# Optimization experiments

Measured on AMD Instinct MI355X. Metric: run time of the kernel, lower is better.

## Reference

```python
import jax, jax.numpy as jnp
import numpy as np

B, E, DM = 2, 1024, 512          # batch, n_edges, d_model
H, DK, DV = 8, 64, 64            # heads, d_k, d_v
MAX_NEIGHBOR = 5                 # == attn_max_dist
LN_EPS = 1e-6
NEG = -1e9


def setup_inputs() -> dict:
    key = jax.random.key(0)
    ks = jax.random.split(key, 9)
    s = 0.02
    return {
        "x": jax.random.normal(ks[0], (B, DM, E, 1), jnp.float32),
        "dist": jax.random.randint(ks[1], (B, E, E), 0, 12, jnp.int32),
        "base_rpr": jax.random.normal(ks[2], (MAX_NEIGHBOR + 1, DK), jnp.float32) * s,
        "w_q": jax.random.normal(ks[3], (DM, H * DK), jnp.float32) * s,
        "w_k": jax.random.normal(ks[4], (DM, H * DK), jnp.float32) * s,
        "w_v": jax.random.normal(ks[5], (DM, H * DV), jnp.float32) * s,
        "w_fc": jax.random.normal(ks[6], (H * DV, DM), jnp.float32) * s,
        "ln_g": jnp.ones((DM,), jnp.float32),
        "ln_b": jnp.zeros((DM,), jnp.float32),
    }


def reference(x, dist, base_rpr, w_q, w_k, w_v, w_fc, ln_g, ln_b):
    temp = jnp.asarray(DK, x.dtype) ** 0.5
    # local-attention mask (dist <= attn_max_dist); all edges valid (same-size meshes)
    mask = dist <= MAX_NEIGHBOR                      # [B,E,E] bool

    s = jnp.transpose(x[..., 0], (0, 2, 1))          # [B,E,DM]
    residual = s

    # LayerNorm applied to q only (as in the torch module)
    mu = s.mean(-1, keepdims=True)
    var = ((s - mu) ** 2).mean(-1, keepdims=True)
    qn = (s - mu) / jnp.sqrt(var + LN_EPS) * ln_g + ln_b

    q = (qn @ w_q).reshape(B, E, H, DK).transpose(0, 2, 1, 3)   # [B,H,E,DK]
    k = (s @ w_k).reshape(B, E, H, DK).transpose(0, 2, 1, 3)
    v = (s @ w_v).reshape(B, E, H, DV).transpose(0, 2, 1, 3)

    # relative-position representations gathered by (clipped) distance
    rpr = base_rpr[jnp.minimum(dist, MAX_NEIGHBOR)]  # [B,E,E,DK]

    qs = q / temp
    attn1 = jnp.einsum("bhid,bhjd->bhij", qs, k)
    attn2 = jnp.einsum("bhid,bijd->bhij", qs, rpr)
    logits = jnp.where(mask[:, None], attn1 + attn2, NEG)
    attn = jax.nn.softmax(logits, axis=-1)           # [B,H,E,E]

    out = jnp.einsum("bhij,bhjd->bhid", attn, v)     # [B,H,E,DV]
    out = out.transpose(0, 2, 1, 3).reshape(B, E, H * DV) @ w_fc + residual
    x_out = out.transpose(0, 2, 1)[..., None]        # [B,DM,E,1]

    mf = mask[:, None].astype(attn.dtype)            # [B,1,E,E]
    attn_per_edge = (attn * mf).sum((1, 2)) / mf.sum((1, 2))  # [B,E]
    return x_out, attn, attn_per_edge
```

## Files before the change

### kernel.cpp

```cpp
#include <hip/hip_runtime.h>

#define NB_B 2
#define NB_E 1024
#define NB_DM 512
#define NB_H 8

typedef __attribute__((ext_vector_type(8))) __bf16 bf16x8;
typedef __attribute__((ext_vector_type(8))) unsigned short u16x8;
typedef __attribute__((ext_vector_type(4))) float f32x4;

static __device__ __forceinline__ float bf2f(unsigned short u){
  union { unsigned int i; float f; } v; v.i = ((unsigned int)u) << 16; return v.f;
}
static __device__ __forceinline__ unsigned short f2bf(float f){
  union { float f; unsigned int i; } v; v.f = f;
  unsigned int r = v.i + 0x7FFFu + ((v.i >> 16) & 1u);
  return (unsigned short)(r >> 16);
}
static __device__ __forceinline__ f32x4 mfma16(bf16x8 a, bf16x8 b, f32x4 c){
  return __builtin_amdgcn_mfma_f32_16x16x32_bf16(a, b, c, 0, 0, 0);
}
static __device__ __forceinline__ float fast_exp2(float x){
#if __has_builtin(__builtin_amdgcn_exp2f)
  return __builtin_amdgcn_exp2f(x);
#else
  return exp2f(x);
#endif
}

__global__ void k_transpose_x(const float* __restrict__ x, unsigned short* __restrict__ s_bf){
  __shared__ float tile[32][33];
  const int b = blockIdx.z;
  const int d0 = blockIdx.y * 32;
  const int e0 = blockIdx.x * 32;
  const int tx = threadIdx.x, ty = threadIdx.y;
  #pragma unroll
  for (int r = 0; r < 4; ++r){
    const int d = d0 + ty + r*8;
    tile[ty + r*8][tx] = x[((size_t)b*NB_DM + d)*NB_E + e0 + tx];
  }
  __syncthreads();
  #pragma unroll
  for (int r = 0; r < 4; ++r){
    const int e = e0 + ty + r*8;
    s_bf[((size_t)b*NB_E + e)*NB_DM + d0 + tx] = f2bf(tile[tx][ty + r*8]);
  }
}

__global__ void k_transpose_w(const float* __restrict__ w0, const float* __restrict__ w1,
                              const float* __restrict__ w2, const float* __restrict__ w3,
                              unsigned short* __restrict__ wT){
  __shared__ float tile[32][33];
  const int which = blockIdx.z;
  const float* w = which==0 ? w0 : which==1 ? w1 : which==2 ? w2 : w3;
  unsigned short* dst = wT + (size_t)which*512*512;
  const int k0 = blockIdx.y*32, n0 = blockIdx.x*32;
  const int tx = threadIdx.x, ty = threadIdx.y;
  #pragma unroll
  for (int r = 0; r < 4; ++r)
    tile[ty + r*8][tx] = w[(size_t)(k0 + ty + r*8)*512 + n0 + tx];
  __syncthreads();
  #pragma unroll
  for (int r = 0; r < 4; ++r)
    dst[(size_t)(n0 + ty + r*8)*512 + k0 + tx] = f2bf(tile[tx][ty + r*8]);
}

__global__ __launch_bounds__(256) void k_ln(const unsigned short* __restrict__ s_bf,
    unsigned short* __restrict__ qn_bf, const float* __restrict__ gg, const float* __restrict__ bb){
  const int row = blockIdx.x*4 + (threadIdx.x >> 6);
  const int l = threadIdx.x & 63;
  const unsigned short* sp = s_bf + (size_t)row*512 + l*8;
  u16x8 v = *(const u16x8*)sp;
  float f[8]; float sum = 0.f, sq = 0.f;
  #pragma unroll
  for (int i = 0; i < 8; ++i){ f[i] = bf2f(v[i]); sum += f[i]; sq += f[i]*f[i]; }
  #pragma unroll
  for (int off = 32; off >= 1; off >>= 1){
    sum += __shfl_xor(sum, off);
    sq  += __shfl_xor(sq, off);
  }
  const float mu  = sum * (1.f/512.f);
  const float var = sq * (1.f/512.f) - mu*mu;
  const float rstd = rsqrtf(var + 1e-6f);
  const float4 g0 = *(const float4*)(gg + l*8);
  const float4 g1 = *(const float4*)(gg + l*8 + 4);
  const float4 b0 = *(const float4*)(bb + l*8);
  const float4 b1 = *(const float4*)(bb + l*8 + 4);
  const float gv[8] = {g0.x,g0.y,g0.z,g0.w,g1.x,g1.y,g1.z,g1.w};
  const float bv[8] = {b0.x,b0.y,b0.z,b0.w,b1.x,b1.y,b1.z,b1.w};
  u16x8 o;
  #pragma unroll
  for (int i = 0; i < 8; ++i) o[i] = f2bf((f[i]-mu)*rstd*gv[i] + bv[i]);
  *(u16x8*)(qn_bf + (size_t)row*512 + l*8) = o;
}

__global__ __launch_bounds__(256) void k_dist(const int* __restrict__ dist,
    unsigned char* __restrict__ d8, int* __restrict__ cnt){
  const int b = blockIdx.y;
  const int i0 = blockIdx.x * 16;
  const int t = threadIdx.x;
  int c0 = 0, c1 = 0, c2 = 0, c3 = 0;
  #pragma unroll 4
  for (int r = 0; r < 16; ++r){
    const int row = i0 + r;
    const int4 d = ((const int4*)(dist + ((size_t)b*NB_E + row)*NB_E))[t];
    uchar4 o;
    o.x = (unsigned char)(d.x <= 5 ? d.x : 6);
    o.y = (unsigned char)(d.y <= 5 ? d.y : 6);
    o.z = (unsigned char)(d.z <= 5 ? d.z : 6);
    o.w = (unsigned char)(d.w <= 5 ? d.w : 6);
    ((uchar4*)(d8 + ((size_t)b*NB_E + row)*NB_E))[t] = o;
    c0 += (d.x <= 5); c1 += (d.y <= 5); c2 += (d.z <= 5); c3 += (d.w <= 5);
  }
  int* cb = cnt + b*NB_E + t*4;
  atomicAdd(cb + 0, c0);
  atomicAdd(cb + 1, c1);
  atomicAdd(cb + 2, c2);
  atomicAdd(cb + 3, c3);
}

__global__ __launch_bounds__(256, 4) void k_gemm_qkv(
    const unsigned short* __restrict__ qn, const unsigned short* __restrict__ s,
    const unsigned short* __restrict__ wT, const float* __restrict__ base_rpr,
    unsigned short* __restrict__ Qb, unsigned short* __restrict__ Kb,
    unsigned short* __restrict__ VTb, float* __restrict__ qr)
{
  const int z = blockIdx.z;
  const unsigned short* A  = (z == 0) ? qn : s;
  const unsigned short* BT = wT + (size_t)z*262144;
  const int tid = threadIdx.x;
  const int l = tid & 63, wv = tid >> 6;
  const int ll = l & 15, lg = l >> 4;
  const int m0 = blockIdx.x*64 + wv*16;
  const int n0 = blockIdx.y*64;
  const unsigned short* arow = A + (size_t)(m0 + ll)*512 + lg*8;
  const unsigned short* brow = BT + (size_t)(n0 + ll)*512 + lg*8;
  f32x4 acc[4];
  #pragma unroll
  for (int nt = 0; nt < 4; ++nt) acc[nt] = (f32x4){0.f,0.f,0.f,0.f};
  bf16x8 a_c = *(const bf16x8*)(arow);
  bf16x8 b_c[4];
  #pragma unroll
  for (int nt = 0; nt < 4; ++nt) b_c[nt] = *(const bf16x8*)(brow + (size_t)nt*8192);
  #pragma unroll
  for (int ks = 0; ks < 16; ++ks){
    const int kn = (ks + 1) & 15;
    bf16x8 a_n = *(const bf16x8*)(arow + kn*32);
    bf16x8 b_n[4];
    #pragma unroll
    for (int nt = 0; nt < 4; ++nt) b_n[nt] = *(const bf16x8*)(brow + (size_t)nt*8192 + kn*32);
    #pragma unroll
    for (int nt = 0; nt < 4; ++nt) acc[nt] = mfma16(a_c, b_c[nt], acc[nt]);
    a_c = a_n;
    #pragma unroll
    for (int nt = 0; nt < 4; ++nt) b_c[nt] = b_n[nt];
  }
  const int rbase = m0 + lg*4;
  const int bidx = rbase >> 10;
  const int e = rbase & 1023;
  const int h = n0 >> 6;
  if (z == 0){
    float rprv[6][4];
    #pragma unroll
    for (int c = 0; c < 6; ++c)
      #pragma unroll
      for (int nt = 0; nt < 4; ++nt)
        rprv[c][nt] = base_rpr[c*64 + nt*16 + ll];
    #pragma unroll
    for (int nt = 0; nt < 4; ++nt){
      const int dk = nt*16 + ll;
      unsigned short* dp = Qb + (((size_t)bidx*NB_H + h)*NB_E + e)*64 + dk;
      #pragma unroll
      for (int r = 0; r < 4; ++r)
        dp[(size_t)r*64] = f2bf(acc[nt][r]*0.125f);
    }
    #pragma unroll
    for (int r = 0; r < 4; ++r){
      #pragma unroll
      for (int c = 0; c < 6; ++c){
        float tv = 0.f;
        #pragma unroll
        for (int nt = 0; nt < 4; ++nt) tv += acc[nt][r]*0.125f*rprv[c][nt];
        tv += __shfl_xor(tv, 1);
        tv += __shfl_xor(tv, 2);
        tv += __shfl_xor(tv, 4);
        tv += __shfl_xor(tv, 8);
        if (ll == 0)
          qr[(((size_t)(bidx*NB_H + h)*NB_E) + e + r)*8 + c] = tv;
      }
    }
  } else if (z == 1){
    #pragma unroll
    for (int nt = 0; nt < 4; ++nt){
      const int dk = nt*16 + ll;
      unsigned short* dp = Kb + (((size_t)bidx*NB_H + h)*NB_E + e)*64 + dk;
      #pragma unroll
      for (int r = 0; r < 4; ++r)
        dp[(size_t)r*64] = f2bf(acc[nt][r]);
    }
  } else {
    #pragma unroll
    for (int nt = 0; nt < 4; ++nt){
      const int dv = nt*16 + ll;
      ushort4 ov;
      ov.x = f2bf(acc[nt][0]); ov.y = f2bf(acc[nt][1]);
      ov.z = f2bf(acc[nt][2]); ov.w = f2bf(acc[nt][3]);
      *(ushort4*)(VTb + (((size_t)bidx*NB_H + h)*64 + dv)*NB_E + e) = ov;
    }
  }
}

__global__ __launch_bounds__(256, 4) void k_fc(
    const unsigned short* __restrict__ A, const unsigned short* __restrict__ BT,
    float* __restrict__ dst_f, const float* __restrict__ resid)
{
  const int tid = threadIdx.x;
  const int l = tid & 63, wv = tid >> 6;
  const int ll = l & 15, lg = l >> 4;
  const int m0 = blockIdx.x*64 + wv*16;
  const int n0 = blockIdx.y*32;
  const unsigned short* arow = A + (size_t)(m0 + ll)*512 + lg*8;
  const unsigned short* brow = BT + (size_t)(n0 + ll)*512 + lg*8;
  f32x4 acc[2];
  acc[0] = (f32x4){0.f,0.f,0.f,0.f};
  acc[1] = (f32x4){0.f,0.f,0.f,0.f};
  bf16x8 a_c = *(const bf16x8*)(arow);
  bf16x8 b_c0 = *(const bf16x8*)(brow);
  bf16x8 b_c1 = *(const bf16x8*)(brow + 8192);
  #pragma unroll
  for (int ks = 0; ks < 16; ++ks){
    const int kn = (ks + 1) & 15;
    bf16x8 a_n  = *(const bf16x8*)(arow + kn*32);
    bf16x8 b_n0 = *(const bf16x8*)(brow + kn*32);
    bf16x8 b_n1 = *(const bf16x8*)(brow + 8192 + kn*32);
    acc[0] = mfma16(a_c, b_c0, acc[0]);
    acc[1] = mfma16(a_c, b_c1, acc[1]);
    a_c = a_n; b_c0 = b_n0; b_c1 = b_n1;
  }
  const int rbase = m0 + lg*4;
  const int bidx = rbase >> 10;
  const int e = rbase & 1023;
  #pragma unroll
  for (int nt = 0; nt < 2; ++nt){
    const int n = n0 + nt*16 + ll;
    const float* xr = resid + ((size_t)bidx*NB_DM + n)*NB_E + e;
    const float4 rv = *(const float4*)xr;
    const float4 ov = make_float4(acc[nt][0]+rv.x, acc[nt][1]+rv.y,
                                  acc[nt][2]+rv.z, acc[nt][3]+rv.w);
    *(float4*)(dst_f + ((size_t)bidx*NB_DM + n)*NB_E + e) = ov;
  }
}

#define D_OFF 1024
#define P_OFF 10240
__global__ __launch_bounds__(512, 8) void k_attn(
    const unsigned short* __restrict__ Q, const unsigned short* __restrict__ K,
    const unsigned short* __restrict__ VT, const float* __restrict__ qr,
    const unsigned char* __restrict__ d8, float* __restrict__ attn_out,
    unsigned short* __restrict__ outb, float* __restrict__ apeacc16)
{
  __shared__ __align__(16) unsigned char smem[26624];
  unsigned short* plds = (unsigned short*)(smem + P_OFF);
  float* qr_l = (float*)smem;
  float* reds = (float*)(smem + 256);

  const int tid = threadIdx.x;
  const int l = tid & 63, w = tid >> 6;
  const int lg = l >> 4, ll = l & 15;
  const int n = blockIdx.x;
  const int m = n >> 3;
  const int bh = (n & 7)*2 + (m >> 7);
  const int b = bh >> 3;
  const int ib = (m & 127) << 3;
  const int j0 = w << 7;

  const unsigned char* d8g = d8 + ((size_t)b*NB_E + ib)*NB_E;
  const int4 dr0 = ((const int4*)d8g)[tid];
  ((int4*)(smem + D_OFF))[tid] = dr0;

  if (tid < 48)
    qr_l[tid] = qr[((size_t)bh*NB_E + ib + (tid/6))*8 + (tid % 6)];

  const unsigned short* Qbp = Q + ((size_t)bh*NB_E + ib)*64;
  bf16x8 qf0 = *(const bf16x8*)(Qbp + (size_t)(ll & 7)*64 + lg*8);
  bf16x8 qf1 = *(const bf16x8*)(Qbp + (size_t)(ll & 7)*64 + 32 + lg*8);

  f32x4 s[8];
  const unsigned short* Kb = K + (size_t)bh*NB_E*64;
  #pragma unroll
  for (int jt = 0; jt < 8; ++jt){
    const size_t krow = (size_t)(j0 + jt*16 + ll)*64;
    bf16x8 k0 = *(const bf16x8*)(Kb + krow + lg*8);
    bf16x8 k1 = *(const bf16x8*)(Kb + krow + 32 + lg*8);
    f32x4 acc = {0.f,0.f,0.f,0.f};
    acc = mfma16(qf0, k0, acc);
    acc = mfma16(qf1, k1, acc);
    s[jt] = acc;
  }
  __syncthreads();

  if (lg < 2){
    float rsum[4] = {0.f, 0.f, 0.f, 0.f};
    #pragma unroll
    for (int jt = 0; jt < 8; ++jt){
      const int j = j0 + jt*16 + ll;
      #pragma unroll
      for (int r = 0; r < 4; ++r){
        const int il = lg*4 + r;
        const unsigned char c = smem[D_OFF + il*1024 + j];
        const float p = (c < 6)
          ? fast_exp2((s[jt][r] + qr_l[il*6 + c]) * 1.4426950408889634f) : 0.f;
        s[jt][r] = p;
        rsum[r] += p;
      }
    }
    #pragma unroll
    for (int r = 0; r < 4; ++r){
      float sum = rsum[r];
      sum += __shfl_xor(sum, 1);
      sum += __shfl_xor(sum, 2);
      sum += __shfl_xor(sum, 4);
      sum += __shfl_xor(sum, 8);
      if (ll == 0) reds[w*8 + lg*4 + r] = sum;
    }
  }
  __syncthreads();

  if (lg < 2){
    float rinv[4];
    #pragma unroll
    for (int r = 0; r < 4; ++r){
      const int il = lg*4 + r;
      float tot = 0.f;
      #pragma unroll
      for (int wv = 0; wv < 8; ++wv) tot += reds[wv*8 + il];
      rinv[r] = 1.0f / (tot + 1e-30f);
    }
    #pragma unroll
    for (int jt = 0; jt < 8; ++jt){
      const int j = j0 + jt*16 + ll;
      float csum = 0.f;
      #pragma unroll
      for (int r = 0; r < 4; ++r){
        const int il = lg*4 + r;
        const float pn = s[jt][r] * rinv[r];
        const int byo = ((il*1024 + j)*2) ^ (il << 4);
        plds[byo >> 1] = f2bf(pn);
        csum += pn;
      }
      csum += __shfl_xor(csum, 16);
      if (lg == 0) atomicAdd(&apeacc16[(bh << 10) + j], csum);
    }
  }
  __syncthreads();

  if (w < 4){
    const unsigned short* Vb = VT + ((size_t)bh*64 + w*16 + ll)*NB_E;
    f32x4 o = {0.f,0.f,0.f,0.f};
    #pragma unroll 4
    for (int kk = 0; kk < 32; ++kk){
      bf16x8 vf = *(const bf16x8*)(Vb + kk*32 + lg*8);
      const int byo = (((ll & 7)*1024 + kk*32 + lg*8)*2) ^ ((ll & 7) << 4);
      bf16x8 p = *(const bf16x8*)(smem + P_OFF + byo);
      o = mfma16(p, vf, o);
    }
    if (lg < 2){
      const int coln = (bh & 7)*64 + w*16 + ll;
      #pragma unroll
      for (int r = 0; r < 4; ++r){
        const int e0 = ib + lg*4 + r;
        outb[((size_t)b*NB_E + e0)*512 + coln] = f2bf(o[r]);
      }
    }
  }

  {
    float* arow = attn_out + ((size_t)bh*NB_E + ib + w)*NB_E;
    #pragma unroll
    for (int c2 = 0; c2 < 4; ++c2){
      const int col = c2*256 + l*4;
      const int byo = ((w*1024 + col)*2) ^ (w << 4);
      const ushort4 pv = *(const ushort4*)(smem + P_OFF + byo);
      f32x4 ov;
      ov[0] = bf2f(pv.x); ov[1] = bf2f(pv.y); ov[2] = bf2f(pv.z); ov[3] = bf2f(pv.w);
      *(f32x4*)(arow + col) = ov;
    }
  }
}

__global__ void k_ape(const float* __restrict__ acc, const int* __restrict__ cnt,
                      float* __restrict__ out){
  const int t = blockIdx.x*256 + threadIdx.x;
  if (t < NB_B*NB_E){
    const int b = t >> 10, j = t & 1023;
    float ssum = 0.f;
    #pragma unroll
    for (int h = 0; h < 8; ++h) ssum += acc[(((b<<3) + h) << 10) + j];
    const int c = cnt[t];
    out[t] = c > 0 ? ssum / (float)c : 0.f;
  }
}

extern "C" void kernel_launch(void* const* d_in, const int* in_sizes, int n_in,
                              void* d_out, int out_size, void* d_ws, size_t ws_size,
                              hipStream_t stream)
{
  const float* x        = (const float*)d_in[0];
  const int*   dist     = (const int*)d_in[1];
  const float* base_rpr = (const float*)d_in[2];
  const float* w_q      = (const float*)d_in[3];
  const float* w_k      = (const float*)d_in[4];
  const float* w_v      = (const float*)d_in[5];
  const float* w_fc     = (const float*)d_in[6];
  const float* ln_g     = (const float*)d_in[7];
  const float* ln_b     = (const float*)d_in[8];

  float* x_out    = (float*)d_out;
  float* attn_out = x_out + (size_t)NB_B*NB_DM*NB_E;
  float* ape_out  = attn_out + (size_t)NB_B*NB_H*NB_E*NB_E;

  unsigned char* ws = (unsigned char*)d_ws;
  unsigned short* s_bf   = (unsigned short*)(ws);
  unsigned short* qn_bf  = (unsigned short*)(ws + 2097152);
  unsigned short* wT     = (unsigned short*)(ws + 4194304);
  unsigned short* Qb     = (unsigned short*)(ws + 6291456);
  unsigned short* Kb     = (unsigned short*)(ws + 8388608);
  unsigned short* VTb    = (unsigned short*)(ws + 10485760);
  unsigned short* outb   = (unsigned short*)(ws + 12582912);
  float*          qr     = (float*)(ws + 14680064);
  unsigned char*  d8     = ws + 15204352;
  int*            cnt    = (int*)(ws + 17301504);
  float*          ape16  = (float*)(ws + 17309696);

  (void)hipMemsetAsync(cnt, 0, 8192 + 65536, stream);

  k_transpose_w<<<dim3(16,16,4), dim3(32,8), 0, stream>>>(w_q, w_k, w_v, w_fc, wT);
  k_transpose_x<<<dim3(32,16,2), dim3(32,8), 0, stream>>>(x, s_bf);
  k_ln<<<dim3(512), dim3(256), 0, stream>>>(s_bf, qn_bf, ln_g, ln_b);
  k_dist<<<dim3(64,2), dim3(256), 0, stream>>>(dist, d8, cnt);

  k_gemm_qkv<<<dim3(32,8,3), dim3(256), 0, stream>>>(qn_bf, s_bf, wT, base_rpr,
                                                     Qb, Kb, VTb, qr);

  k_attn<<<dim3(2048), dim3(512), 0, stream>>>(Qb, Kb, VTb, qr, d8,
                                               attn_out, outb, ape16);

  k_fc<<<dim3(32,16), dim3(256), 0, stream>>>(outb, wT + 786432, x_out, x);
  k_ape<<<dim3(8), dim3(256), 0, stream>>>(ape16, cnt, ape_out);
}
```

Baseline: 149.5 us.

## Process 16-row attention tiles in persistent blocks and replace ape atomics with partial buffer

The attention kernel now handles 16 query rows per tile instead of 8, so all 16 MFMA rows are used. It runs as a persistent grid of 512 blocks that each loop over two tiles. Per-column attention sums are written to a partial-sum buffer that reuses the s_bf workspace region, replacing global atomics, and a new reduction kernel combines them. Waves 4-7 write the attn output while waves 0-3 do the PV matmul. LDS use doubles and occupancy bounds drop. A tiny kernel replaces the memset.

```diff
diff --git a/kernel.cpp b/kernel.cpp
--- a/kernel.cpp
+++ b/kernel.cpp
@@ -26,6 +26,10 @@
 #else
   return exp2f(x);
 #endif
+}
+
+__global__ __launch_bounds__(512) void k_zero(int* __restrict__ cnt){
+  ((int4*)cnt)[threadIdx.x] = make_int4(0,0,0,0);
 }
 
 __global__ void k_transpose_x(const float* __restrict__ x, unsigned short* __restrict__ s_bf){
@@ -251,57 +255,60 @@
   }
 }
 
-#define D_OFF 1024
-#define P_OFF 10240
-__global__ __launch_bounds__(512, 8) void k_attn(
+#define D_OFF 2048
+#define P_OFF 18432
+__global__ __launch_bounds__(512, 4) void k_attn(
     const unsigned short* __restrict__ Q, const unsigned short* __restrict__ K,
     const unsigned short* __restrict__ VT, const float* __restrict__ qr,
     const unsigned char* __restrict__ d8, float* __restrict__ attn_out,
-    unsigned short* __restrict__ outb, float* __restrict__ apeacc16)
+    unsigned short* __restrict__ outb, float* __restrict__ apeP)
 {
-  __shared__ __align__(16) unsigned char smem[26624];
+  __shared__ __align__(16) unsigned char smem[51200];
   unsigned short* plds = (unsigned short*)(smem + P_OFF);
   float* qr_l = (float*)smem;
-  float* reds = (float*)(smem + 256);
+  float* reds = (float*)(smem + 512);
 
   const int tid = threadIdx.x;
   const int l = tid & 63, w = tid >> 6;
   const int lg = l >> 4, ll = l & 15;
-  const int n = blockIdx.x;
-  const int m = n >> 3;
-  const int bh = (n & 7)*2 + (m >> 7);
-  const int b = bh >> 3;
-  const int ib = (m & 127) << 3;
   const int j0 = w << 7;
 
-  const unsigned char* d8g = d8 + ((size_t)b*NB_E + ib)*NB_E;
-  const int4 dr0 = ((const int4*)d8g)[tid];
-  ((int4*)(smem + D_OFF))[tid] = dr0;
-
-  if (tid < 48)
-    qr_l[tid] = qr[((size_t)bh*NB_E + ib + (tid/6))*8 + (tid % 6)];
-
-  const unsigned short* Qbp = Q + ((size_t)bh*NB_E + ib)*64;
-  bf16x8 qf0 = *(const bf16x8*)(Qbp + (size_t)(ll & 7)*64 + lg*8);
-  bf16x8 qf1 = *(const bf16x8*)(Qbp + (size_t)(ll & 7)*64 + 32 + lg*8);
-
-  f32x4 s[8];
-  const unsigned short* Kb = K + (size_t)bh*NB_E*64;
-  #pragma unroll
-  for (int jt = 0; jt < 8; ++jt){
-    const size_t krow = (size_t)(j0 + jt*16 + ll)*64;
-    bf16x8 k0 = *(const bf16x8*)(Kb + krow + lg*8);
-    bf16x8 k1 = *(const bf16x8*)(Kb + krow + 32 + lg*8);
-    f32x4 acc = {0.f,0.f,0.f,0.f};
-    acc = mfma16(qf0, k0, acc);
-    acc = mfma16(qf1, k1, acc);
-    s[jt] = acc;
-  }
-  __syncthreads();
-
-  if (lg < 2){
+  #pragma unroll 1
+  for (int t = blockIdx.x; t < 1024; t += 512){
+    const int m = t >> 3;
+    const int bh = (t & 7)*2 + (m >> 6);
+    const int b = bh >> 3;
+    const int it = m & 63;
+    const int ib = it << 4;
+
+    const unsigned char* d8g = d8 + ((size_t)b*NB_E + ib)*NB_E;
+    const int4 dr0 = ((const int4*)d8g)[tid];
+    const int4 dr1 = ((const int4*)(d8g + 8192))[tid];
+    ((int4*)(smem + D_OFF))[tid] = dr0;
+    ((int4*)(smem + D_OFF + 8192))[tid] = dr1;
+    if (tid < 96)
+      qr_l[tid] = qr[((size_t)bh*NB_E + ib + (tid/6))*8 + (tid % 6)];
+
+    const unsigned short* Qbp = Q + ((size_t)bh*NB_E + ib)*64;
+    const bf16x8 qf0 = *(const bf16x8*)(Qbp + (size_t)ll*64 + lg*8);
+    const bf16x8 qf1 = *(const bf16x8*)(Qbp + (size_t)ll*64 + 32 + lg*8);
+
+    f32x4 s[8];
+    const unsigned short* Kb = K + (size_t)bh*NB_E*64;
+    #pragma unroll 2
+    for (int jt = 0; jt < 8; ++jt){
+      const size_t krow = (size_t)(j0 + jt*16 + ll)*64;
+      const bf16x8 k0 = *(const bf16x8*)(Kb + krow + lg*8);
+      const bf16x8 k1 = *(const bf16x8*)(Kb + krow + 32 + lg*8);
+      f32x4 acc = {0.f,0.f,0.f,0.f};
+      acc = mfma16(qf0, k0, acc);
+      acc = mfma16(qf1, k1, acc);
+      s[jt] = acc;
+    }
+    __syncthreads();
+
     float rsum[4] = {0.f, 0.f, 0.f, 0.f};
-    #pragma unroll
+    #pragma unroll 2
     for (int jt = 0; jt < 8; ++jt){
       const int j = j0 + jt*16 + ll;
       #pragma unroll
@@ -321,22 +328,21 @@
       sum += __shfl_xor(sum, 2);
       sum += __shfl_xor(sum, 4);
       sum += __shfl_xor(sum, 8);
-      if (ll == 0) reds[w*8 + lg*4 + r] = sum;
-    }
-  }
-  __syncthreads();
-
-  if (lg < 2){
+      if (ll == 0) reds[w*16 + lg*4 + r] = sum;
+    }
+    __syncthreads();
     float rinv[4];
     #pragma unroll
     for (int r = 0; r < 4; ++r){
       const int il = lg*4 + r;
       float tot = 0.f;
       #pragma unroll
-      for (int wv = 0; wv < 8; ++wv) tot += reds[wv*8 + il];
+      for (int wv = 0; wv < 8; ++wv) tot += reds[wv*16 + il];
       rinv[r] = 1.0f / (tot + 1e-30f);
     }
-    #pragma unroll
+
+    float* apeRow = apeP + (((size_t)bh*64 + it) << 10);
+    #pragma unroll 2
     for (int jt = 0; jt < 8; ++jt){
       const int j = j0 + jt*16 + ll;
       float csum = 0.f;
@@ -344,60 +350,75 @@
       for (int r = 0; r < 4; ++r){
         const int il = lg*4 + r;
         const float pn = s[jt][r] * rinv[r];
-        const int byo = ((il*1024 + j)*2) ^ (il << 4);
+        const int byo = ((il*1024 + j)*2) ^ ((il & 7) << 4);
         plds[byo >> 1] = f2bf(pn);
         csum += pn;
       }
       csum += __shfl_xor(csum, 16);
-      if (lg == 0) atomicAdd(&apeacc16[(bh << 10) + j], csum);
-    }
-  }
-  __syncthreads();
-
-  if (w < 4){
-    const unsigned short* Vb = VT + ((size_t)bh*64 + w*16 + ll)*NB_E;
-    f32x4 o = {0.f,0.f,0.f,0.f};
-    #pragma unroll 4
-    for (int kk = 0; kk < 32; ++kk){
-      bf16x8 vf = *(const bf16x8*)(Vb + kk*32 + lg*8);
-      const int byo = (((ll & 7)*1024 + kk*32 + lg*8)*2) ^ ((ll & 7) << 4);
-      bf16x8 p = *(const bf16x8*)(smem + P_OFF + byo);
-      o = mfma16(p, vf, o);
-    }
-    if (lg < 2){
+      csum += __shfl_xor(csum, 32);
+      if (l < 16) apeRow[j0 + jt*16 + l] = csum;
+    }
+    __syncthreads();
+
+    if (w < 4){
+      const unsigned short* Vb = VT + ((size_t)bh*64 + w*16 + ll)*NB_E;
+      f32x4 o = {0.f,0.f,0.f,0.f};
+      #pragma unroll 4
+      for (int kk = 0; kk < 32; ++kk){
+        const bf16x8 vf = *(const bf16x8*)(Vb + kk*32 + lg*8);
+        const int byo = ((ll*2048 + (kk*32 + lg*8)*2)) ^ ((ll & 7) << 4);
+        const bf16x8 p = *(const bf16x8*)(smem + P_OFF + byo);
+        o = mfma16(p, vf, o);
+      }
       const int coln = (bh & 7)*64 + w*16 + ll;
       #pragma unroll
       for (int r = 0; r < 4; ++r){
         const int e0 = ib + lg*4 + r;
         outb[((size_t)b*NB_E + e0)*512 + coln] = f2bf(o[r]);
       }
-    }
-  }
-
-  {
-    float* arow = attn_out + ((size_t)bh*NB_E + ib + w)*NB_E;
-    #pragma unroll
-    for (int c2 = 0; c2 < 4; ++c2){
-      const int col = c2*256 + l*4;
-      const int byo = ((w*1024 + col)*2) ^ (w << 4);
-      const ushort4 pv = *(const ushort4*)(smem + P_OFF + byo);
-      f32x4 ov;
-      ov[0] = bf2f(pv.x); ov[1] = bf2f(pv.y); ov[2] = bf2f(pv.z); ov[3] = bf2f(pv.w);
-      *(f32x4*)(arow + col) = ov;
-    }
-  }
-}
-
-__global__ void k_ape(const float* __restrict__ acc, const int* __restrict__ cnt,
-                      float* __restrict__ out){
-  const int t = blockIdx.x*256 + threadIdx.x;
-  if (t < NB_B*NB_E){
-    const int b = t >> 10, j = t & 1023;
-    float ssum = 0.f;
-    #pragma unroll
-    for (int h = 0; h < 8; ++h) ssum += acc[(((b<<3) + h) << 10) + j];
-    const int c = cnt[t];
-    out[t] = c > 0 ? ssum / (float)c : 0.f;
+    } else {
+      #pragma unroll
+      for (int r2 = 0; r2 < 4; ++r2){
+        const int il = (w - 4)*4 + r2;
+        float* arow = attn_out + ((size_t)bh*NB_E + ib + il)*NB_E;
+        #pragma unroll
+        for (int c2 = 0; c2 < 4; ++c2){
+          const int col = c2*256 + l*4;
+          const int byo = ((il*1024 + col)*2) ^ ((il & 7) << 4);
+          const ushort4 pv = *(const ushort4*)(smem + P_OFF + byo);
+          f32x4 ov;
+          ov[0] = bf2f(pv.x); ov[1] = bf2f(pv.y); ov[2] = bf2f(pv.z); ov[3] = bf2f(pv.w);
+          *(f32x4*)(arow + col) = ov;
+        }
+      }
+    }
+    __syncthreads();
+  }
+}
+
+__global__ __launch_bounds__(256) void k_apered(const float* __restrict__ apeP,
+    const int* __restrict__ cnt, float* __restrict__ out)
+{
+  __shared__ float psum[8][32];
+  const int b = blockIdx.x;
+  const int jg = blockIdx.y;
+  const int t = threadIdx.x;
+  const int col = jg*32 + (t & 31);
+  const int rseg = t >> 5;
+  const float* base = apeP + ((size_t)b*512)*1024 + col;
+  float acc = 0.f;
+  #pragma unroll 8
+  for (int i = 0; i < 64; ++i)
+    acc += base[(size_t)(rseg + 8*i) << 10];
+  psum[rseg][t & 31] = acc;
+  __syncthreads();
+  if (t < 32){
+    float sv = 0.f;
+    #pragma unroll
+    for (int r2 = 0; r2 < 8; ++r2) sv += psum[r2][t];
+    const int j = jg*32 + t;
+    const int c = cnt[b*NB_E + j];
+    out[b*NB_E + j] = c > 0 ? sv / (float)c : 0.f;
   }
 }
 
@@ -422,6 +443,7 @@
   unsigned char* ws = (unsigned char*)d_ws;
   unsigned short* s_bf   = (unsigned short*)(ws);
   unsigned short* qn_bf  = (unsigned short*)(ws + 2097152);
+  float*          apeP   = (float*)(ws);
   unsigned short* wT     = (unsigned short*)(ws + 4194304);
   unsigned short* Qb     = (unsigned short*)(ws + 6291456);
   unsigned short* Kb     = (unsigned short*)(ws + 8388608);
@@ -430,9 +452,8 @@
   float*          qr     = (float*)(ws + 14680064);
   unsigned char*  d8     = ws + 15204352;
   int*            cnt    = (int*)(ws + 17301504);
-  float*          ape16  = (float*)(ws + 17309696);
-
-  (void)hipMemsetAsync(cnt, 0, 8192 + 65536, stream);
+
+  k_zero<<<dim3(1), dim3(512), 0, stream>>>(cnt);
 
   k_transpose_w<<<dim3(16,16,4), dim3(32,8), 0, stream>>>(w_q, w_k, w_v, w_fc, wT);
   k_transpose_x<<<dim3(32,16,2), dim3(32,8), 0, stream>>>(x, s_bf);
@@ -442,9 +463,9 @@
   k_gemm_qkv<<<dim3(32,8,3), dim3(256), 0, stream>>>(qn_bf, s_bf, wT, base_rpr,
                                                      Qb, Kb, VTb, qr);
 
-  k_attn<<<dim3(2048), dim3(512), 0, stream>>>(Qb, Kb, VTb, qr, d8,
-                                               attn_out, outb, ape16);
+  k_attn<<<dim3(512), dim3(512), 0, stream>>>(Qb, Kb, VTb, qr, d8,
+                                              attn_out, outb, apeP);
 
   k_fc<<<dim3(32,16), dim3(256), 0, stream>>>(outb, wT + 786432, x_out, x);
-  k_ape<<<dim3(8), dim3(256), 0, stream>>>(ape16, cnt, ape_out);
-}
+  k_apered<<<dim3(2,32), dim3(256), 0, stream>>>(apeP, cnt, ape_out);
+}
```

After: 128.8 us. 1.16x faster.
